# Kernel optimization log

Hardware: AMD Instinct MI355X
Metric: run time of the kernel (lower is better)

## Reference

```python
import jax, jax.numpy as jnp
import numpy as np

FIRE_RATE = 0.5
ANGLE = 0.0


def _kernels(angle):
    dx = np.outer([1, 2, 1], [-1, 0, 1]) / 8.0
    dy = dx.T
    dlap = np.array([[1, 2, 1], [2, -12, 2], [1, 2, 1]]) / 8.0
    dlap2 = np.array([[0, 1, 0], [1, -4, 1], [0, 1, 0]]) / 8.0
    c = np.cos(angle * np.pi / 180.0)
    s = np.sin(angle * np.pi / 180.0)
    w1 = c * dx - s * dy
    w2 = s * dx + c * dy
    return [jnp.asarray(k, jnp.float32) for k in (w1, w2, dlap, dlap2)]


def _dwconv(x, k):
    # x: [B,H,W,C], k: [3,3] applied depthwise (same kernel every channel)
    C = x.shape[-1]
    rhs = jnp.broadcast_to(k[:, :, None, None], (3, 3, 1, C))
    return jax.lax.conv_general_dilated(
        x, rhs, window_strides=(1, 1), padding='SAME',
        dimension_numbers=('NHWC', 'HWIO', 'NHWC'), feature_group_count=C)


def _alive(x):
    # 3x3 max-pool (stride 1, SAME) over alpha channel (index 3) > 0.1
    a = jax.lax.reduce_window(x[..., 3:4], -jnp.inf, jax.lax.max,
                              (1, 3, 3, 1), (1, 1, 1, 1), 'SAME')
    return a > 0.1


def _update(x, W0, b0, W1, key):
    pre_life = _alive(x)                                  # [B,H,W,1] bool
    ks = _kernels(ANGLE)
    y = jnp.concatenate([x] + [_dwconv(x, k) for k in ks], axis=-1)  # [B,H,W,5C]
    h = jax.nn.relu(y @ W0 + b0)                          # [B,H,W,hidden]
    d = h @ W1                                            # [B,H,W,C]
    stoch = (jax.random.uniform(key, d.shape[:3] + (1,)) > FIRE_RATE).astype(d.dtype)
    x = x + d * stoch
    life = (pre_life & _alive(x)).astype(x.dtype)
    return x * life


def setup_inputs() -> dict:
    key = jax.random.key(0)
    k1, k2, k3, k4 = jax.random.split(key, 4)
    B, H, W, C, HID = 8, 256, 256, 16, 128
    return {
        'x': jax.random.normal(k1, (B, H, W, C), jnp.float32),
        'W0': jax.random.normal(k2, (5 * C, HID), jnp.float32) * 0.05,
        'b0': jax.random.normal(k3, (HID,), jnp.float32) * 0.05,
        'W1': jax.random.normal(k4, (HID, C), jnp.float32) * 0.05,
        'steps': 2,
    }


def reference(x, W0, b0, W1, steps):
    base = jax.random.key(42)
    for step in range(steps):
        x = _update(x, W0, b0, W1, jax.random.fold_in(base, step))
    return x
```

## Files before the change

kernel.cpp:

```cpp
#include <hip/hip_runtime.h>
#include <stdint.h>

#define BB 8
#define HH 256
#define WW 256
#define CC 16
#define HID 128
#define NPIX (BB*HH*WW)
#define MTILE 64
#define NBLK (NPIX/MTILE)

typedef _Float16 h8 __attribute__((ext_vector_type(8)));
typedef __fp16   fp16v2 __attribute__((ext_vector_type(2)));
typedef float    f4 __attribute__((ext_vector_type(4)));

#define YPK_HI   0
#define YPK_MID  3328
#define HS_OFF   0
#define CTR_OFF  8704
#define FIRE_OFF 9984
#define LDS_DW   10048

__host__ __device__ __forceinline__ uint32_t rotl32(uint32_t x, int r) {
  return (x << r) | (x >> (32 - r));
}

__host__ __device__ inline void threefry2x32(uint32_t k0, uint32_t k1,
                                             uint32_t x0, uint32_t x1,
                                             uint32_t& o0, uint32_t& o1) {
  const uint32_t ks2 = k0 ^ k1 ^ 0x1BD11BDAu;
  x0 += k0; x1 += k1;
#define TF_R4(a,b,c,d) \
  x0 += x1; x1 = rotl32(x1,(a)); x1 ^= x0; \
  x0 += x1; x1 = rotl32(x1,(b)); x1 ^= x0; \
  x0 += x1; x1 = rotl32(x1,(c)); x1 ^= x0; \
  x0 += x1; x1 = rotl32(x1,(d)); x1 ^= x0;
  TF_R4(13,15,26,6)   x0 += k1;  x1 += ks2 + 1u;
  TF_R4(17,29,16,24)  x0 += ks2; x1 += k0 + 2u;
  TF_R4(13,15,26,6)   x0 += k0;  x1 += k1 + 3u;
  TF_R4(17,29,16,24)  x0 += k1;  x1 += ks2 + 4u;
  TF_R4(13,15,26,6)   x0 += ks2; x1 += k0 + 5u;
#undef TF_R4
  o0 = x0; o1 = x1;
}

__device__ __forceinline__ void split2(float a, float b, uint32_t& hi, uint32_t& mid) {
  _Float16 ha = (_Float16)a, hb = (_Float16)b;
  union { _Float16 h[2]; uint32_t u; } ph;
  ph.h[0] = ha; ph.h[1] = hb; hi = ph.u;
  float ra = a - (float)ha, rb = b - (float)hb;
  union { fp16v2 h; uint32_t u; } pu;
  pu.h = __builtin_amdgcn_cvt_pkrtz(ra, rb);
  mid = pu.u;
}

__global__ __launch_bounds__(256)
void prep_frags(const float* __restrict__ W0g, const float* __restrict__ W1g,
                uint32_t* __restrict__ W0F, uint32_t* __restrict__ W1F) {
  const int tid = blockIdx.x * 256 + threadIdx.x;
  for (int idx = tid; idx < 6144; idx += gridDim.x * 256) {
    const int r = idx & 3, l = (idx >> 2) & 63, ks = (idx >> 8) % 3, n = idx / 768;
    const int g = l >> 4, c = l & 15;
    const int k0 = 32 * ks + 8 * g + 2 * r;
    const int hid = 16 * n + c;
    const float a = (k0     < 80) ? W0g[k0 * HID + hid]       : 0.f;
    const float b = (k0 + 1 < 80) ? W0g[(k0 + 1) * HID + hid] : 0.f;
    uint32_t hi, mid; split2(a, b, hi, mid);
    W0F[(size_t)(((n * 3 + ks) * 2 + 0) * 64 + l) * 4 + r] = hi;
    W0F[(size_t)(((n * 3 + ks) * 2 + 1) * 64 + l) * 4 + r] = mid;
  }
  for (int idx = tid; idx < 1024; idx += gridDim.x * 256) {
    const int r = idx & 3, l = (idx >> 2) & 63, ks = idx >> 8;
    const int g = l >> 4, c = l & 15;
    float va[2];
#pragma unroll
    for (int h = 0; h < 2; ++h) {
      const int khat = 2 * g + 16 * (r & 1) + 8 * h + (r >> 1);
      va[h] = W1g[(size_t)(32 * ks + khat) * CC + c];
    }
    uint32_t hi, mid; split2(va[0], va[1], hi, mid);
    W1F[(size_t)((ks * 2 + 0) * 64 + l) * 4 + r] = hi;
    W1F[(size_t)((ks * 2 + 1) * 64 + l) * 4 + r] = mid;
  }
}

__global__ __launch_bounds__(256, 4)
void step_fused(const float* __restrict__ xin,
                const uint32_t* __restrict__ W0F,
                const uint32_t* __restrict__ W1F,
                const float* __restrict__ b0g,
                float* __restrict__ xn,
                float* __restrict__ alpha_out,
                unsigned char* __restrict__ prelife,
                uint32_t k0, uint32_t k1) {
  __shared__ uint32_t LDSU[LDS_DW];
  float* const LDSF = (float*)LDSU;

  const int t    = threadIdx.x;
  const int blk  = blockIdx.x;
  const int lane = t & 63;
  const int w    = __builtin_amdgcn_readfirstlane(t >> 6);
  const int g    = lane >> 4;
  const int c15  = lane & 15;

  uint4 BH[2][2], BM[2][2];
#pragma unroll
  for (int nl = 0; nl < 2; ++nl) {
    const int n = 2 * w + nl;
    BH[0][nl] = *(const uint4*)(W0F + (size_t)(((n * 3 + 0) * 2 + 0) * 64 + lane) * 4);
    BM[0][nl] = *(const uint4*)(W0F + (size_t)(((n * 3 + 0) * 2 + 1) * 64 + lane) * 4);
  }
  const float bv0 = b0g[16 * (2 * w + 0) + c15];
  const float bv1 = b0g[16 * (2 * w + 1) + c15];

  const int px  = t >> 2;
  const int c4  = (t & 3) * 4;
  const int gpx = blk * MTILE + px;
  const int bi  = gpx >> 16;
  const int ij  = gpx & 0xFFFF;
  const int ic  = ij >> 8;
  const int jc  = ij & 0xFF;

  const float DXW[3][3] = {{-0.125f, 0.0f, 0.125f},
                           {-0.25f,  0.0f, 0.25f },
                           {-0.125f, 0.0f, 0.125f}};
  const float DYW[3][3] = {{-0.125f, -0.25f, -0.125f},
                           { 0.0f,    0.0f,   0.0f  },
                           { 0.125f,  0.25f,  0.125f}};
  const float LPW[3][3] = {{0.125f, 0.25f, 0.125f},
                           {0.25f, -1.5f,  0.25f },
                           {0.125f, 0.25f, 0.125f}};
  const float L2W[3][3] = {{0.0f,   0.125f, 0.0f  },
                           {0.125f, -0.5f,  0.125f},
                           {0.0f,   0.125f, 0.0f  }};

  float ctr[4] = {0,0,0,0};
  float adx[4] = {0,0,0,0};
  float ady[4] = {0,0,0,0};
  float alp[4] = {0,0,0,0};
  float al2[4] = {0,0,0,0};
  float amax = 0.0f;

  const float* xb = xin + (size_t)bi * (HH * WW * CC);
#pragma unroll
  for (int di = -1; di <= 1; ++di) {
#pragma unroll
    for (int dj = -1; dj <= 1; ++dj) {
      const int ii = ic + di, jj = jc + dj;
      const bool ok = ((unsigned)ii < (unsigned)HH) && ((unsigned)jj < (unsigned)WW);
      float4 p = make_float4(0.f, 0.f, 0.f, 0.f);
      if (ok) p = *(const float4*)(xb + ((size_t)(ii * WW + jj) * CC + c4));
      const float wdx = DXW[di+1][dj+1], wdy = DYW[di+1][dj+1];
      const float wlp = LPW[di+1][dj+1], wl2 = L2W[di+1][dj+1];
      const float pv[4] = {p.x, p.y, p.z, p.w};
#pragma unroll
      for (int q = 0; q < 4; ++q) {
        if (di == 0 && dj == 0) ctr[q] = pv[q];
        if (wdx != 0.f) adx[q] = fmaf(pv[q], wdx, adx[q]);
        if (wdy != 0.f) ady[q] = fmaf(pv[q], wdy, ady[q]);
        if (wlp != 0.f) alp[q] = fmaf(pv[q], wlp, alp[q]);
        if (wl2 != 0.f) al2[q] = fmaf(pv[q], wl2, al2[q]);
      }
      if (c4 == 0) amax = fmaxf(amax, p.w);
    }
  }

  {
    const int q2 = c4 >> 1;
#define WRYPK(grp, A) do { \
    uint32_t h0_, m0_, h1_, m1_; \
    split2(A[0], A[1], h0_, m0_); split2(A[2], A[3], h1_, m1_); \
    const int kk_ = 8 * (grp) + q2; \
    *(uint2*)&LDSU[YPK_HI  + px * 52 + kk_] = make_uint2(h0_, h1_); \
    *(uint2*)&LDSU[YPK_MID + px * 52 + kk_] = make_uint2(m0_, m1_); \
  } while (0)
    WRYPK(0, ctr); WRYPK(1, adx); WRYPK(2, ady); WRYPK(3, alp); WRYPK(4, al2);
#undef WRYPK
  }
#pragma unroll
  for (int j = 0; j < 4; ++j) {
    const int pos = t * 4 + j;
    const int plane = pos >> 9, rem = pos & 511;
    LDSU[plane * 3328 + (rem >> 3) * 52 + 40 + (rem & 7)] = 0u;
  }
  *(f4*)&LDSU[CTR_OFF + px * 20 + c4] = (f4){ctr[0], ctr[1], ctr[2], ctr[3]};
  if (c4 == 0) prelife[gpx] = (amax > 0.1f) ? 1 : 0;
  if (t < 64) {
    uint32_t lo, hi2;
    threefry2x32(k0, k1, 0u, (uint32_t)(blk * MTILE + t), lo, hi2);
    const uint32_t bits = lo ^ hi2;
    const float u = __uint_as_float((bits >> 9) | 0x3f800000u) - 1.0f;
    LDSF[FIRE_OFF + t] = (u > 0.5f) ? 1.0f : 0.0f;
  }

  __syncthreads();

  f4 C1[4][2];
#pragma unroll
  for (int m = 0; m < 4; ++m) {
    C1[m][0] = (f4){bv0, bv0, bv0, bv0};
    C1[m][1] = (f4){bv1, bv1, bv1, bv1};
  }

#define LOADB(par, kss) do { \
  _Pragma("unroll") for (int nl_ = 0; nl_ < 2; ++nl_) { \
    const int n_ = 2 * w + nl_; \
    BH[par][nl_] = *(const uint4*)(W0F + (size_t)(((n_ * 3 + (kss)) * 2 + 0) * 64 + lane) * 4); \
    BM[par][nl_] = *(const uint4*)(W0F + (size_t)(((n_ * 3 + (kss)) * 2 + 1) * 64 + lane) * 4); \
  } } while (0)

  const int abase = c15 * 52 + 4 * g;
#pragma unroll
  for (int ks = 0; ks < 3; ++ks) {
    if (ks == 0) LOADB(1, 1);
    if (ks == 1) LOADB(0, 2);
    const int cur = ks & 1;
#pragma unroll
    for (int m = 0; m < 4; ++m) {
      const uint4 uh = *(const uint4*)&LDSU[YPK_HI  + abase + m * 832 + 16 * ks];
      const uint4 um = *(const uint4*)&LDSU[YPK_MID + abase + m * 832 + 16 * ks];
      const h8 ah = __builtin_bit_cast(h8, uh);
      const h8 am = __builtin_bit_cast(h8, um);
#pragma unroll
      for (int nl = 0; nl < 2; ++nl) {
        const h8 bh = __builtin_bit_cast(h8, BH[cur][nl]);
        const h8 bm = __builtin_bit_cast(h8, BM[cur][nl]);
        C1[m][nl] = __builtin_amdgcn_mfma_f32_16x16x32_f16(ah, bh, C1[m][nl], 0, 0, 0);
        C1[m][nl] = __builtin_amdgcn_mfma_f32_16x16x32_f16(am, bh, C1[m][nl], 0, 0, 0);
        C1[m][nl] = __builtin_amdgcn_mfma_f32_16x16x32_f16(ah, bm, C1[m][nl], 0, 0, 0);
      }
    }
  }
#undef LOADB

  __syncthreads();

#pragma unroll
  for (int m = 0; m < 4; ++m)
#pragma unroll
    for (int nl = 0; nl < 2; ++nl) {
      f4 hv = C1[m][nl];
      hv.x = fmaxf(hv.x, 0.f); hv.y = fmaxf(hv.y, 0.f);
      hv.z = fmaxf(hv.z, 0.f); hv.w = fmaxf(hv.w, 0.f);
      const int hid = 16 * (2 * w + nl) + c15;
      *(f4*)&LDSU[HS_OFF + hid * 68 + 16 * m + 4 * g] = hv;
    }

  uint4 W1H[4], W1M[4];
#pragma unroll
  for (int ks = 0; ks < 4; ++ks) {
    W1H[ks] = *(const uint4*)(W1F + (size_t)((ks * 2 + 0) * 64 + lane) * 4);
    W1M[ks] = *(const uint4*)(W1F + (size_t)((ks * 2 + 1) * 64 + lane) * 4);
  }

  __syncthreads();

  f4 C2 = (f4){0.f, 0.f, 0.f, 0.f};
  const int A2 = 136 * g + 16 * w + c15;
#pragma unroll
  for (int ks = 0; ks < 4; ++ks) {
    uint32_t ph[4], pm[4];
#pragma unroll
    for (int r = 0; r < 4; ++r) {
      const int K0 = 16 * (r & 1) + (r >> 1);
      const float a = LDSF[A2 + 68 * (32 * ks + K0)];
      const float b = LDSF[A2 + 68 * (32 * ks + K0 + 8)];
      split2(a, b, ph[r], pm[r]);
    }
    const uint4 uh = make_uint4(ph[0], ph[1], ph[2], ph[3]);
    const uint4 um = make_uint4(pm[0], pm[1], pm[2], pm[3]);
    const h8 bh = __builtin_bit_cast(h8, uh);
    const h8 bm = __builtin_bit_cast(h8, um);
    const h8 ah = __builtin_bit_cast(h8, W1H[ks]);
    const h8 am = __builtin_bit_cast(h8, W1M[ks]);
    C2 = __builtin_amdgcn_mfma_f32_16x16x32_f16(ah, bh, C2, 0, 0, 0);
    C2 = __builtin_amdgcn_mfma_f32_16x16x32_f16(am, bh, C2, 0, 0, 0);
    C2 = __builtin_amdgcn_mfma_f32_16x16x32_f16(ah, bm, C2, 0, 0, 0);
  }

  {
    const int pxt  = 16 * w + c15;
    const int gpx2 = blk * MTILE + pxt;
    const f4 ctr4 = *(const f4*)&LDSU[CTR_OFF + pxt * 20 + 4 * g];
    const float fire01 = LDSF[FIRE_OFF + pxt];
    f4 xv;
    xv.x = fmaf(C2.x, fire01, ctr4.x);
    xv.y = fmaf(C2.y, fire01, ctr4.y);
    xv.z = fmaf(C2.z, fire01, ctr4.z);
    xv.w = fmaf(C2.w, fire01, ctr4.w);
    *(f4*)&xn[(size_t)gpx2 * CC + 4 * g] = xv;
    if (g == 0) alpha_out[gpx2] = xv.w;
  }
}

__global__ __launch_bounds__(256)
void life_mask(const float* __restrict__ xn,
               const float* __restrict__ alpha,
               const unsigned char* __restrict__ prelife,
               float* __restrict__ out) {
  const int idx = blockIdx.x * 256 + threadIdx.x;
  const int b  = idx >> 16;
  const int ij = idx & 0xFFFF;
  const int i  = ij >> 8;
  const int j  = ij & 0xFF;

  const float* ab = alpha + (size_t)b * (HH * WW);
  float amax = 0.0f;
#pragma unroll
  for (int di = -1; di <= 1; ++di) {
    const int ii = i + di;
    if ((unsigned)ii >= (unsigned)HH) continue;
#pragma unroll
    for (int dj = -1; dj <= 1; ++dj) {
      const int jj = j + dj;
      if ((unsigned)jj >= (unsigned)WW) continue;
      amax = fmaxf(amax, ab[(size_t)ii * WW + jj]);
    }
  }
  const bool life = (prelife[idx] != 0) && (amax > 0.1f);

  const float4* src = (const float4*)(xn + (size_t)idx * CC);
  float4* dst = (float4*)(out + (size_t)idx * CC);
  if (life) {
    dst[0] = src[0]; dst[1] = src[1]; dst[2] = src[2]; dst[3] = src[3];
  } else {
    const float4 z = make_float4(0.0f, 0.0f, 0.0f, 0.0f);
    dst[0] = z; dst[1] = z; dst[2] = z; dst[3] = z;
  }
}

extern "C" void kernel_launch(void* const* d_in, const int* in_sizes, int n_in,
                              void* d_out, int out_size, void* d_ws, size_t ws_size,
                              hipStream_t stream) {
  (void)in_sizes; (void)n_in; (void)out_size; (void)ws_size;
  const float* x  = (const float*)d_in[0];
  const float* W0 = (const float*)d_in[1];
  const float* b0 = (const float*)d_in[2];
  const float* W1 = (const float*)d_in[3];
  float* out = (float*)d_out;

  float* xn = (float*)d_ws;
  float* alpha = xn + (size_t)NPIX * CC;
  unsigned char* mask = (unsigned char*)(alpha + NPIX);
  uint32_t* W0F = (uint32_t*)(mask + NPIX);
  uint32_t* W1F = W0F + 12288;

  prep_frags<<<24, 256, 0, stream>>>(W0, W1, W0F, W1F);

  const int steps = 2;
  for (int s = 0; s < steps; ++s) {
    uint32_t fk0, fk1;
    threefry2x32(0u, 42u, 0u, (uint32_t)s, fk0, fk1);
    const float* xin = (s == 0) ? x : out;
    step_fused<<<NBLK, 256, 0, stream>>>(xin, W0F, W1F, b0, xn, alpha, mask, fk0, fk1);
    life_mask<<<NPIX / 256, 256, 0, stream>>>(xn, alpha, mask, out);
  }
}
```

Before: 234.8 us.

## Fuse step-one life mask into step-two stencil load and zero-only final pass

Removes the intermediate life_mask pass between the two steps. The second step_fused launch now recomputes the step-one life mask on the fly from the previous alpha plane and prelife mask, using a small LDS halo tile, and multiplies the loaded neighbours by it. The final pass only writes zeros for dead pixels instead of copying the whole state, which saves a full read and write of the 16-channel tensor. The cost is extra syncthreads, LDS halo work in the step kernel, and double-buffered alpha and mask arrays.

Result: faster. 217.4 us (-7.4%).

```diff
diff --git a/kernel.cpp b/kernel.cpp
--- a/kernel.cpp
+++ b/kernel.cpp
@@ -14,12 +14,14 @@
 typedef __fp16   fp16v2 __attribute__((ext_vector_type(2)));
 typedef float    f4 __attribute__((ext_vector_type(4)));
 
-#define YPK_HI   0
-#define YPK_MID  3328
-#define HS_OFF   0
-#define CTR_OFF  8704
-#define FIRE_OFF 9984
-#define LDS_DW   10048
+#define YPK_HI     0
+#define YPK_MID    3328
+#define HS_OFF     0
+#define ALPHA5_OFF 6656
+#define LIFE_OFF   6996
+#define CTR_OFF    8704
+#define FIRE_OFF   9984
+#define LDS_DW     10048
 
 __host__ __device__ __forceinline__ uint32_t rotl32(uint32_t x, int r) {
   return (x << r) | (x >> (32 - r));
@@ -89,10 +91,12 @@
                 const uint32_t* __restrict__ W0F,
                 const uint32_t* __restrict__ W1F,
                 const float* __restrict__ b0g,
+                const float* __restrict__ aPrev,
+                const unsigned char* __restrict__ mPrev,
                 float* __restrict__ xn,
                 float* __restrict__ alpha_out,
                 unsigned char* __restrict__ prelife,
-                uint32_t k0, uint32_t k1) {
+                uint32_t k0, uint32_t k1, int apply_life) {
   __shared__ uint32_t LDSU[LDS_DW];
   float* const LDSF = (float*)LDSU;
 
@@ -113,13 +117,43 @@
   const float bv0 = b0g[16 * (2 * w + 0) + c15];
   const float bv1 = b0g[16 * (2 * w + 1) + c15];
 
+  const int base_ = blk * MTILE;
+  const int bi    = base_ >> 16;
+  const int rc    = base_ & 0xFFFF;
+  const int ic    = rc >> 8;
+  const int jc0   = rc & 0xFF;
+
+  if (apply_life) {
+    const float* ap = aPrev + (size_t)bi * (HH * WW);
+    for (int it = t; it < 340; it += 256) {
+      const int r = it / 68, c = it - r * 68;
+      const int ii = ic - 2 + r, jj = jc0 - 2 + c;
+      float v = 0.f;
+      if ((unsigned)ii < (unsigned)HH && (unsigned)jj < (unsigned)WW)
+        v = ap[ii * WW + jj];
+      LDSF[ALPHA5_OFF + it] = v;
+    }
+    __syncthreads();
+    if (t < 198) {
+      const int r = t / 66, xx = t - r * 66;
+      const float* a0 = &LDSF[ALPHA5_OFF + r * 68 + xx];
+      const float m0 = fmaxf(fmaxf(a0[0],   a0[1]),   a0[2]);
+      const float m1 = fmaxf(fmaxf(a0[68],  a0[69]),  a0[70]);
+      const float m2 = fmaxf(fmaxf(a0[136], a0[137]), a0[138]);
+      const float mm = fmaxf(fmaxf(m0, m1), m2);
+      const int ii = ic - 1 + r, jj = jc0 - 1 + xx;
+      int pl = 0;
+      if ((unsigned)ii < (unsigned)HH && (unsigned)jj < (unsigned)WW)
+        pl = mPrev[(size_t)bi * (HH * WW) + ii * WW + jj];
+      LDSF[LIFE_OFF + t] = (pl && mm > 0.1f) ? 1.0f : 0.0f;
+    }
+    __syncthreads();
+  }
+
   const int px  = t >> 2;
   const int c4  = (t & 3) * 4;
-  const int gpx = blk * MTILE + px;
-  const int bi  = gpx >> 16;
-  const int ij  = gpx & 0xFFFF;
-  const int ic  = ij >> 8;
-  const int jc  = ij & 0xFF;
+  const int gpx = base_ + px;
+  const int jc  = jc0 + px;
 
   const float DXW[3][3] = {{-0.125f, 0.0f, 0.125f},
                            {-0.25f,  0.0f, 0.25f },
@@ -150,6 +184,10 @@
       const bool ok = ((unsigned)ii < (unsigned)HH) && ((unsigned)jj < (unsigned)WW);
       float4 p = make_float4(0.f, 0.f, 0.f, 0.f);
       if (ok) p = *(const float4*)(xb + ((size_t)(ii * WW + jj) * CC + c4));
+      if (apply_life) {
+        const float lf = LDSF[LIFE_OFF + (di + 1) * 66 + (px + dj + 1)];
+        p.x *= lf; p.y *= lf; p.z *= lf; p.w *= lf;
+      }
       const float wdx = DXW[di+1][dj+1], wdy = DYW[di+1][dj+1];
       const float wlp = LPW[di+1][dj+1], wl2 = L2W[di+1][dj+1];
       const float pv[4] = {p.x, p.y, p.z, p.w};
@@ -187,7 +225,7 @@
   if (c4 == 0) prelife[gpx] = (amax > 0.1f) ? 1 : 0;
   if (t < 64) {
     uint32_t lo, hi2;
-    threefry2x32(k0, k1, 0u, (uint32_t)(blk * MTILE + t), lo, hi2);
+    threefry2x32(k0, k1, 0u, (uint32_t)(base_ + t), lo, hi2);
     const uint32_t bits = lo ^ hi2;
     const float u = __uint_as_float((bits >> 9) | 0x3f800000u) - 1.0f;
     LDSF[FIRE_OFF + t] = (u > 0.5f) ? 1.0f : 0.0f;
@@ -280,7 +318,7 @@
 
   {
     const int pxt  = 16 * w + c15;
-    const int gpx2 = blk * MTILE + pxt;
+    const int gpx2 = base_ + pxt;
     const f4 ctr4 = *(const f4*)&LDSU[CTR_OFF + pxt * 20 + 4 * g];
     const float fire01 = LDSF[FIRE_OFF + pxt];
     f4 xv;
@@ -294,10 +332,9 @@
 }
 
 __global__ __launch_bounds__(256)
-void life_mask(const float* __restrict__ xn,
-               const float* __restrict__ alpha,
-               const unsigned char* __restrict__ prelife,
-               float* __restrict__ out) {
+void life_final(float* __restrict__ out,
+                const float* __restrict__ alpha,
+                const unsigned char* __restrict__ prelife) {
   const int idx = blockIdx.x * 256 + threadIdx.x;
   const int b  = idx >> 16;
   const int ij = idx & 0xFFFF;
@@ -318,13 +355,9 @@
     }
   }
   const bool life = (prelife[idx] != 0) && (amax > 0.1f);
-
-  const float4* src = (const float4*)(xn + (size_t)idx * CC);
-  float4* dst = (float4*)(out + (size_t)idx * CC);
-  if (life) {
-    dst[0] = src[0]; dst[1] = src[1]; dst[2] = src[2]; dst[3] = src[3];
-  } else {
+  if (!life) {
     const float4 z = make_float4(0.0f, 0.0f, 0.0f, 0.0f);
+    float4* dst = (float4*)(out + (size_t)idx * CC);
     dst[0] = z; dst[1] = z; dst[2] = z; dst[3] = z;
   }
 }
@@ -340,19 +373,21 @@
   float* out = (float*)d_out;
 
   float* xn = (float*)d_ws;
-  float* alpha = xn + (size_t)NPIX * CC;
-  unsigned char* mask = (unsigned char*)(alpha + NPIX);
-  uint32_t* W0F = (uint32_t*)(mask + NPIX);
+  float* alphaA = xn + (size_t)NPIX * CC;
+  float* alphaB = alphaA + NPIX;
+  unsigned char* maskA = (unsigned char*)(alphaB + NPIX);
+  unsigned char* maskB = maskA + NPIX;
+  uint32_t* W0F = (uint32_t*)(maskB + NPIX);
   uint32_t* W1F = W0F + 12288;
 
   prep_frags<<<24, 256, 0, stream>>>(W0, W1, W0F, W1F);
 
-  const int steps = 2;
-  for (int s = 0; s < steps; ++s) {
-    uint32_t fk0, fk1;
-    threefry2x32(0u, 42u, 0u, (uint32_t)s, fk0, fk1);
-    const float* xin = (s == 0) ? x : out;
-    step_fused<<<NBLK, 256, 0, stream>>>(xin, W0F, W1F, b0, xn, alpha, mask, fk0, fk1);
-    life_mask<<<NPIX / 256, 256, 0, stream>>>(xn, alpha, mask, out);
-  }
-}
+  uint32_t fk0, fk1;
+  threefry2x32(0u, 42u, 0u, 0u, fk0, fk1);
+  step_fused<<<NBLK, 256, 0, stream>>>(x, W0F, W1F, b0, alphaA, maskA,
+                                       xn, alphaA, maskA, fk0, fk1, 0);
+  threefry2x32(0u, 42u, 0u, 1u, fk0, fk1);
+  step_fused<<<NBLK, 256, 0, stream>>>(xn, W0F, W1F, b0, alphaA, maskA,
+                                       out, alphaB, maskB, fk0, fk1, 1);
+  life_final<<<NPIX / 256, 256, 0, stream>>>(out, alphaB, maskB);
+}
```
